# Kernel tuning notes

Hardware: AMD Instinct MI355X
Metric: run time of the kernel (lower is better)

Reference implementation:

```python
import jax, jax.numpy as jnp
import numpy as np
from jax import lax

TOTAL_STEPS = 100
BETA_0 = 0.1
BETA_1 = 20.0


def setup_inputs() -> dict:
    key = jax.random.key(0)
    k1, k2 = jax.random.split(key)
    x = jax.random.normal(k1, (64, 256, 64), dtype=jnp.float32)
    noise = jax.random.normal(k2, (TOTAL_STEPS, 64, 256, 64), dtype=jnp.float32)
    return {"x": x, "noise": noise}


def reference(x, noise):
    # VP-SDE Euler-Maruyama forward diffusion, matching forward_sample.
    S = TOTAL_STEPS
    dt = jnp.float32(1.0 / S)
    sqrt_dt = jnp.sqrt(dt)
    # torch loop uses t in [1..S] and computes coefficients at (t-1)/S
    norm_t = (jnp.arange(S, dtype=jnp.float32)) / S  # (t-1)/S for t=1..S

    def step(x_prev, inp):
        nt, n = inp
        beta_t = BETA_0 + nt * (BETA_1 - BETA_0)
        drift = -0.5 * beta_t * x_prev
        x_t = x_prev + drift * dt + jnp.sqrt(beta_t) * n * sqrt_dt
        return x_t, x_t

    _, traj = lax.scan(step, x, (norm_t, noise))  # traj: (S, N, L, D)
    return jnp.concatenate([x[None], traj], axis=0)  # (S+1, N, L, D)
```

## Files before the change

### kernel.cpp

```cpp
#include <hip/hip_runtime.h>
#include <math.h>


#define S_STEPS 100
#define U 5
#define NW (S_STEPS / U)

typedef float f32x4 __attribute__((ext_vector_type(4)));

__global__ __launch_bounds__(256) void vpsde_fwd_kernel(
    const f32x4* __restrict__ x,
    const f32x4* __restrict__ noise,
    f32x4* __restrict__ out,
    int ne4)
{
    __shared__ float s_a[S_STEPS];
    __shared__ float s_b[S_STEPS];

    const int tid = threadIdx.x;
    if (tid < S_STEPS) {
        const float dt = 0.01f;
        float nt_ = (float)tid * dt;
        float beta = 0.1f + nt_ * 19.9f;
        s_a[tid] = 1.0f - 0.5f * beta * dt;
        s_b[tid] = sqrtf(beta) * 0.1f;
    }
    __syncthreads();

    const int idx = blockIdx.x * blockDim.x + tid;
    if (idx >= ne4) return;

    const f32x4* np_ = noise + idx;
    f32x4* op_ = out + idx;

    f32x4 xv = x[idx];
    __builtin_nontemporal_store(xv, op_);

    f32x4 A[U], B[U];

    auto loadw = [&](f32x4* buf, int w0) {
        #pragma unroll
        for (int k = 0; k < U; ++k)
            buf[k] = np_[(size_t)(w0 + k) * ne4];
    };
    auto consume = [&](const f32x4* buf, int w0) {
        #pragma unroll
        for (int k = 0; k < U; ++k) {
            const int t = w0 + k;
            const float a = s_a[t];
            const float b = s_b[t];
            xv = a * xv + b * buf[k];
            __builtin_nontemporal_store(xv, op_ + (size_t)(t + 1) * ne4);
        }
    };

    loadw(A, 0);
    for (int w = 0; w < NW; w += 2) {
        loadw(B, (w + 1) * U);
        consume(A, w * U);
        if (w + 2 < NW) loadw(A, (w + 2) * U);
        consume(B, (w + 1) * U);
    }
}

extern "C" void kernel_launch(void* const* d_in, const int* in_sizes, int n_in,
                              void* d_out, int out_size, void* d_ws, size_t ws_size,
                              hipStream_t stream) {
    const float* x     = (const float*)d_in[0];
    const float* noise = (const float*)d_in[1];
    float* out         = (float*)d_out;

    const int ne  = in_sizes[0];
    const int ne4 = ne / 4;

    const int block = 256;
    const int grid  = (ne4 + block - 1) / block;

    vpsde_fwd_kernel<<<grid, block, 0, stream>>>(
        (const f32x4*)x, (const f32x4*)noise, (f32x4*)out, ne4);
}
```

Before: 190.5 us.

## Process two vectors per thread with rotating four-stage noise prefetch

Each thread now handles two float4 columns, and the grid is halved to ne4/512 blocks. The time loop is restructured into a rolling four-deep software pipeline: each step is consumed and its buffer immediately refilled with a nontemporal load, replacing the previous double-buffered five-step windows. The aim is to keep a steady stream of memory requests in flight with fewer threads and to bypass cache on the streamed noise. The bounds check is removed, so the kernel assumes ne4 is a multiple of 512. The smaller grid also reduces the number of waves available to hide latency.

```diff
diff --git a/kernel.cpp b/kernel.cpp
--- a/kernel.cpp
+++ b/kernel.cpp
@@ -3,8 +3,7 @@
 
 
 #define S_STEPS 100
-#define U 5
-#define NW (S_STEPS / U)
+#define DEPTH 4
 
 typedef float f32x4 __attribute__((ext_vector_type(4)));
 
@@ -27,40 +26,49 @@
     }
     __syncthreads();
 
-    const int idx = blockIdx.x * blockDim.x + tid;
-    if (idx >= ne4) return;
+    const int wid  = tid >> 6;
+    const int lane = tid & 63;
 
-    const f32x4* np_ = noise + idx;
-    f32x4* op_ = out + idx;
+    const size_t base = (size_t)blockIdx.x * 512 + (size_t)wid * 128 + lane;
 
-    f32x4 xv = x[idx];
-    __builtin_nontemporal_store(xv, op_);
+    const f32x4* gl = noise + base;
+    f32x4*       st = out + base + ne4;
 
-    f32x4 A[U], B[U];
+    f32x4 xv0 = x[base];
+    f32x4 xv1 = x[base + 64];
+    __builtin_nontemporal_store(xv0, out + base);
+    __builtin_nontemporal_store(xv1, out + base + 64);
 
-    auto loadw = [&](f32x4* buf, int w0) {
-        #pragma unroll
-        for (int k = 0; k < U; ++k)
-            buf[k] = np_[(size_t)(w0 + k) * ne4];
+    int t = 0;
+
+    f32x4 A[2], B[2], C[2], Dq[2];
+
+    auto loadp = [&](f32x4* buf) {
+        buf[0] = __builtin_nontemporal_load(gl);
+        buf[1] = __builtin_nontemporal_load(gl + 64);
+        gl += ne4;
     };
-    auto consume = [&](const f32x4* buf, int w0) {
-        #pragma unroll
-        for (int k = 0; k < U; ++k) {
-            const int t = w0 + k;
-            const float a = s_a[t];
-            const float b = s_b[t];
-            xv = a * xv + b * buf[k];
-            __builtin_nontemporal_store(xv, op_ + (size_t)(t + 1) * ne4);
-        }
+    auto consume = [&](const f32x4* buf) {
+        const float a = s_a[t];
+        const float b = s_b[t];
+        xv0 = a * xv0 + b * buf[0];
+        xv1 = a * xv1 + b * buf[1];
+        __builtin_nontemporal_store(xv0, st);
+        __builtin_nontemporal_store(xv1, st + 64);
+        st += ne4;
+        ++t;
     };
 
-    loadw(A, 0);
-    for (int w = 0; w < NW; w += 2) {
-        loadw(B, (w + 1) * U);
-        consume(A, w * U);
-        if (w + 2 < NW) loadw(A, (w + 2) * U);
-        consume(B, (w + 1) * U);
+    loadp(A); loadp(B); loadp(C); loadp(Dq);
+
+    #pragma unroll 1
+    for (int cyc = 0; cyc < (S_STEPS / DEPTH) - 1; ++cyc) {
+        consume(A);  loadp(A);
+        consume(B);  loadp(B);
+        consume(C);  loadp(C);
+        consume(Dq); loadp(Dq);
     }
+    consume(A); consume(B); consume(C); consume(Dq);
 }
 
 extern "C" void kernel_launch(void* const* d_in, const int* in_sizes, int n_in,
@@ -74,7 +82,7 @@
     const int ne4 = ne / 4;
 
     const int block = 256;
-    const int grid  = (ne4 + block - 1) / block;
+    const int grid  = ne4 / 512;
 
     vpsde_fwd_kernel<<<grid, block, 0, stream>>>(
         (const f32x4*)x, (const f32x4*)noise, (f32x4*)out, ne4);
```

New measurement: 164.2 us. -13.8%, faster.
